# Kernel optimization log

Hardware: AMD Instinct MI355X
Metric: run time of the kernel (lower is better)

Reference implementation:

```python
import jax, jax.numpy as jnp
import numpy as np

N_HEADS = 16

def setup_inputs() -> dict:
    key = jax.random.key(0)
    ks = jax.random.split(key, 6)
    B, T, C = 8, 1024, 1024
    x = jax.random.normal(ks[0], (B, T, C), dtype=jnp.float32)
    s = 0.02
    Wk = jax.random.normal(ks[1], (C, C), dtype=jnp.float32) * s
    Wq = jax.random.normal(ks[2], (C, C), dtype=jnp.float32) * s
    Wv = jax.random.normal(ks[3], (C, C), dtype=jnp.float32) * s
    Wp = jax.random.normal(ks[4], (C, C), dtype=jnp.float32) * s
    bp = jax.random.normal(ks[5], (C,), dtype=jnp.float32) * s
    return {"x": x, "Wk": Wk, "Wq": Wq, "Wv": Wv, "Wp": Wp, "bp": bp}


def reference(x, Wk, Wq, Wv, Wp, bp):
    B, T, C = x.shape
    D = C // N_HEADS
    # torch Linear: y = x @ W^T
    def heads(W):
        h = (x @ W.T).reshape(B, T, N_HEADS, D)
        return jnp.transpose(h, (0, 2, 1, 3))  # [B,H,T,D]
    k, q, v = heads(Wk), heads(Wq), heads(Wv)
    # NOTE: source computes k @ q^T (rows index keys, cols index queries)
    att = jnp.einsum('bhid,bhjd->bhij', k, q) * (D ** -0.5)
    mask = jnp.tril(jnp.ones((T, T), dtype=bool))  # masked_fill where mask==0
    att = jnp.where(mask, att, -jnp.inf)
    att = jax.nn.softmax(att, axis=-1)
    y = jnp.einsum('bhij,bhjd->bhid', att, v)  # [B,H,T,D]
    y = jnp.transpose(y, (0, 2, 1, 3)).reshape(B, T, C)
    return y @ Wp.T + bp
```

## Files before the change

### kernel.cpp

```cpp
#include <hip/hip_runtime.h>
#include <hip/hip_bf16.h>


typedef __attribute__((ext_vector_type(8))) short short8;
typedef __attribute__((ext_vector_type(8))) unsigned short ushort8;
typedef __attribute__((ext_vector_type(4))) unsigned short ushort4_t;
typedef __attribute__((ext_vector_type(4))) unsigned int uintx4;
typedef __attribute__((ext_vector_type(4))) float floatx4;

#define LOG2E 1.44269504088896f

__device__ __forceinline__ unsigned short f2bf(float f) {
  unsigned int u = __float_as_uint(f);
  u += 0x7FFFu + ((u >> 16) & 1u);
  return (unsigned short)(u >> 16);
}

__device__ __forceinline__ unsigned int pack2bf(float lo, float hi) {
  return (unsigned int)f2bf(lo) | ((unsigned int)f2bf(hi) << 16);
}

__device__ __forceinline__ void gload_lds16(const void* g, void* l) {
  __builtin_amdgcn_global_load_lds(
      (const __attribute__((address_space(1))) unsigned int*)g,
      (__attribute__((address_space(3))) unsigned int*)l, 16, 0, 0);
}

__global__ __launch_bounds__(256) void cast_all_kernel(
    const float* __restrict__ x, const float* __restrict__ Wk,
    const float* __restrict__ Wq, const float* __restrict__ Wv,
    const float* __restrict__ Wp, unsigned short* __restrict__ xb,
    unsigned short* __restrict__ wb) {
  int idx = blockIdx.x * 256 + threadIdx.x;
  for (int i = idx; i < 1572864; i += 2048 * 256) {
    const float* src;
    unsigned short* dst;
    if (i < 1048576) {
      src = x + (size_t)i * 8;
      dst = xb + (size_t)i * 8;
    } else {
      int j = i - 1048576;
      int sel = j >> 17;
      int o = (j & 131071) * 8;
      const float* wsrc = sel == 0 ? Wk : sel == 1 ? Wq : sel == 2 ? Wv : Wp;
      src = wsrc + o;
      dst = wb + (size_t)sel * 1048576 + o;
    }
    const float4* p = reinterpret_cast<const float4*>(src);
    float4 a = p[0], b = p[1];
    ushort8 r;
    r[0] = f2bf(a.x); r[1] = f2bf(a.y); r[2] = f2bf(a.z); r[3] = f2bf(a.w);
    r[4] = f2bf(b.x); r[5] = f2bf(b.y); r[6] = f2bf(b.z); r[7] = f2bf(b.w);
    *reinterpret_cast<ushort8*>(dst) = r;
  }
}

template <int MODE, int NB>
__global__ __launch_bounds__(256) void gemm3_kernel(
    const unsigned short* __restrict__ A, const unsigned short* __restrict__ Bb,
    unsigned short* __restrict__ outb, float* __restrict__ outf,
    const float* __restrict__ bias) {
  const int tid = threadIdx.x;
  const int lane = tid & 63;
  const int w = tid >> 6;
  const int wr = w >> 1, wc = w & 1;
  const int g = lane >> 4, r = lane & 15;

  constexpr int NWG = NB * 64;
  constexpr int CPX = NWG / 8;
  const int bid = blockIdx.x;
  const int wgid = (bid & 7) * CPX + (bid >> 3);
  const int mb = wgid / NB, nb = wgid % NB;
  const int m0 = mb * 128, n0 = nb * 128;

  __shared__ unsigned short sA[3][128 * 32];
  __shared__ unsigned short sB[3][128 * 32];

  floatx4 acc[4][4];
#pragma unroll
  for (int i = 0; i < 4; ++i)
#pragma unroll
    for (int j = 0; j < 4; ++j) acc[i][j] = (floatx4)0.0f;

  const int srow = w * 16 + (lane >> 2);
  const int sc = (lane & 3) ^ ((lane >> 2) & 3);
  const char* gA0 = (const char*)(A + (size_t)(m0 + srow) * 1024) + sc * 16;
  const char* gA1 = (const char*)(A + (size_t)(m0 + 64 + srow) * 1024) + sc * 16;
  const char* gB0 = (const char*)(Bb + (size_t)(n0 + srow) * 1024) + sc * 16;
  const char* gB1 = (const char*)(Bb + (size_t)(n0 + 64 + srow) * 1024) + sc * 16;

  auto stage = [&](int bsel, int kt) {
    const size_t off = (size_t)kt * 64;
    gload_lds16(gA0 + off, &sA[bsel][(w * 16) * 32]);
    gload_lds16(gA1 + off, &sA[bsel][(64 + w * 16) * 32]);
    gload_lds16(gB0 + off, &sB[bsel][(w * 16) * 32]);
    gload_lds16(gB1 + off, &sB[bsel][(64 + w * 16) * 32]);
  };

  stage(0, 0);
  stage(1, 1);
  asm volatile("s_waitcnt vmcnt(4)" ::: "memory");
  __builtin_amdgcn_sched_barrier(0);
  __builtin_amdgcn_s_barrier();

  int bcur = 0;
  for (int kt = 0; kt < 32; ++kt) {
    if (kt < 30) {
      stage(bcur == 0 ? 2 : bcur - 1, kt + 2);
      asm volatile("s_waitcnt vmcnt(8)" ::: "memory");
    } else if (kt == 30) {
      asm volatile("s_waitcnt vmcnt(4)" ::: "memory");
    } else {
      asm volatile("s_waitcnt vmcnt(0)" ::: "memory");
    }
    __builtin_amdgcn_sched_barrier(0);

    short8 aF[4], bF[4];
#pragma unroll
    for (int mf = 0; mf < 4; ++mf) {
      const int row = wr * 64 + mf * 16 + r;
      aF[mf] = *reinterpret_cast<const short8*>(
          &sA[bcur][row * 32 + ((g ^ (r & 3)) * 8)]);
    }
#pragma unroll
    for (int nf = 0; nf < 4; ++nf) {
      const int row = wc * 64 + nf * 16 + r;
      bF[nf] = *reinterpret_cast<const short8*>(
          &sB[bcur][row * 32 + ((g ^ (r & 3)) * 8)]);
    }
#pragma unroll
    for (int mf = 0; mf < 4; ++mf)
#pragma unroll
      for (int nf = 0; nf < 4; ++nf)
        acc[mf][nf] = __builtin_amdgcn_mfma_f32_16x16x32_bf16(
            aF[mf], bF[nf], acc[mf][nf], 0, 0, 0);

    asm volatile("s_waitcnt lgkmcnt(0)" ::: "memory");
    __builtin_amdgcn_sched_barrier(0);
    __builtin_amdgcn_s_barrier();
    bcur = (bcur == 2) ? 0 : bcur + 1;
  }

  if (MODE == 0) {
    const int zB = n0 >> 10;
    unsigned short* outz = outb + (size_t)zB * 8388608;
    if (zB == 2) {
#pragma unroll
      for (int mf = 0; mf < 4; ++mf)
#pragma unroll
        for (int nf = 0; nf < 4; ++nf) {
          int m = m0 + wr * 64 + mf * 16 + g * 4;
          int nn = n0 + wc * 64 + nf * 16 + r;
          int b = m >> 10, t = m & 1023, h = (nn & 1023) >> 6, d = nn & 63;
          ushort4_t pk;
          pk[0] = f2bf(acc[mf][nf][0]); pk[1] = f2bf(acc[mf][nf][1]);
          pk[2] = f2bf(acc[mf][nf][2]); pk[3] = f2bf(acc[mf][nf][3]);
          *reinterpret_cast<ushort4_t*>(
              &outz[((size_t)((b * 16 + h) * 64 + d)) * 1024 + t]) = pk;
        }
    } else {
#pragma unroll
      for (int mf = 0; mf < 4; ++mf)
#pragma unroll
        for (int nf = 0; nf < 4; ++nf)
#pragma unroll
          for (int q = 0; q < 4; ++q) {
            int m = m0 + wr * 64 + mf * 16 + g * 4 + q;
            int nn = n0 + wc * 64 + nf * 16 + r;
            int b = m >> 10, t = m & 1023, h = (nn & 1023) >> 6, d = nn & 63;
            outz[(size_t)((b * 16 + h) * 1024 + t) * 64 + d] = f2bf(acc[mf][nf][q]);
          }
    }
  } else {
#pragma unroll
    for (int mf = 0; mf < 4; ++mf)
#pragma unroll
      for (int nf = 0; nf < 4; ++nf) {
        int nn = n0 + wc * 64 + nf * 16 + r;
        float bv = bias[nn];
#pragma unroll
        for (int q = 0; q < 4; ++q) {
          int m = m0 + wr * 64 + mf * 16 + g * 4 + q;
          outf[(size_t)m * 1024 + nn] = acc[mf][nf][q] + bv;
        }
      }
  }
}

__device__ __forceinline__ void softmax_pv_tile(
    floatx4 (&sT)[4], const unsigned short* __restrict__ Vb,
    floatx4 (&accYT)[4], float& m_run, float& l_run,
    int g, int r, int j0, int i_lane, bool diag) {
#pragma unroll
  for (int jf = 0; jf < 4; ++jf)
#pragma unroll
    for (int q = 0; q < 4; ++q) {
      float v = sT[jf][q] * 0.125f;
      if (diag && (j0 + jf * 16 + g * 4 + q > i_lane)) v = -1e30f;
      sT[jf][q] = v;
    }
  float mx = sT[0][0];
#pragma unroll
  for (int jf = 0; jf < 4; ++jf)
#pragma unroll
    for (int q = 0; q < 4; ++q) mx = fmaxf(mx, sT[jf][q]);
  mx = fmaxf(mx, __shfl_xor(mx, 16));
  mx = fmaxf(mx, __shfl_xor(mx, 32));
  float mnew = fmaxf(m_run, mx);
  float corr = exp2f((m_run - mnew) * LOG2E);
  m_run = mnew;
  float ssum = 0.0f;
#pragma unroll
  for (int jf = 0; jf < 4; ++jf)
#pragma unroll
    for (int q = 0; q < 4; ++q) {
      float p = exp2f((sT[jf][q] - mnew) * LOG2E);
      sT[jf][q] = p;
      ssum += p;
    }
  ssum += __shfl_xor(ssum, 16);
  ssum += __shfl_xor(ssum, 32);
  l_run = l_run * corr + ssum;
#pragma unroll
  for (int df = 0; df < 4; ++df) accYT[df] *= corr;
  unsigned int pk[4][2];
#pragma unroll
  for (int jf = 0; jf < 4; ++jf) {
    pk[jf][0] = pack2bf(sT[jf][0], sT[jf][1]);
    pk[jf][1] = pack2bf(sT[jf][2], sT[jf][3]);
  }
  short8 bP[2];
#pragma unroll
  for (int s = 0; s < 2; ++s) {
    uintx4 wd;
#pragma unroll
    for (int w_ = 0; w_ < 4; ++w_) {
      int src = (((g & 1) * 2 + (w_ >> 1)) << 4) + r;
      unsigned int t0 = (unsigned int)__shfl((int)pk[2 * s][w_ & 1], src);
      unsigned int t1 = (unsigned int)__shfl((int)pk[2 * s + 1][w_ & 1], src);
      wd[w_] = (g & 2) ? t1 : t0;
    }
    bP[s] = __builtin_bit_cast(short8, wd);
  }
  __builtin_amdgcn_s_setprio(1);
#pragma unroll
  for (int df = 0; df < 4; ++df) {
#pragma unroll
    for (int s = 0; s < 2; ++s) {
      short8 av = *reinterpret_cast<const short8*>(
          &Vb[(df * 16 + r) * 64 + ((s * 32 + g * 8) ^ ((r & 7) * 8))]);
      accYT[df] = __builtin_amdgcn_mfma_f32_16x16x32_bf16(av, bP[s], accYT[df], 0, 0, 0);
    }
  }
  __builtin_amdgcn_s_setprio(0);
}

__global__ __launch_bounds__(256, 4) void attn_kernel(
    const unsigned short* __restrict__ kqv, unsigned short* __restrict__ y) {
  const int tid = threadIdx.x;
  const int lane = tid & 63;
  const int w = tid >> 6;
  const int g = lane >> 4, r = lane & 15;
  const int bh = blockIdx.y;
  const int z = blockIdx.x;
  const int itA = z, itB = 15 - z;
  const int iwA = itA * 64 + w * 16;
  const int iwB = itB * 64 + w * 16;

  const unsigned short* Kh = kqv + (size_t)bh * 65536;
  const unsigned short* Qh = kqv + 8388608u + (size_t)bh * 65536;
  const unsigned short* Vt = kqv + 16777216u + (size_t)bh * 65536;

  __shared__ unsigned short Qs[2][64 * 64];
  __shared__ unsigned short Vs[2][64 * 64];

  short8 bKA[2], bKB[2];
#pragma unroll
  for (int s = 0; s < 2; ++s) {
    bKA[s] = *reinterpret_cast<const short8*>(&Kh[(size_t)(iwA + r) * 64 + s * 32 + g * 8]);
    bKB[s] = *reinterpret_cast<const short8*>(&Kh[(size_t)(iwB + r) * 64 + s * 32 + g * 8]);
  }

  floatx4 accA[4], accB[4];
#pragma unroll
  for (int df = 0; df < 4; ++df) { accA[df] = (floatx4)0.0f; accB[df] = (floatx4)0.0f; }
  float mA = -1e30f, lA = 0.0f, mB = -1e30f, lB = 0.0f;

  auto stage = [&](int bsel, int jts) {
    const int j0s = jts * 64;
    const int c = lane & 7;
#pragma unroll
    for (int u = 0; u < 2; ++u) {
      const int R = w * 16 + u * 8 + (lane >> 3);
      const int cc = c ^ (R & 7);
      gload_lds16(&Qh[(size_t)(j0s + R) * 64 + cc * 8], &Qs[bsel][(w * 16 + u * 8) * 64]);
      gload_lds16(&Vt[(size_t)R * 1024 + j0s + cc * 8], &Vs[bsel][(w * 16 + u * 8) * 64]);
    }
  };

  int buf = 0;
  stage(0, 0);
  __syncthreads();

  for (int jt = 0; jt <= itB; ++jt) {
    const int j0 = jt * 64;
    if (jt < itB) stage(buf ^ 1, jt + 1);

    const unsigned short* Qb = &Qs[buf][0];
    const unsigned short* Vb = &Vs[buf][0];

    floatx4 sT[4];
    __builtin_amdgcn_s_setprio(1);
#pragma unroll
    for (int jf = 0; jf < 4; ++jf) {
      sT[jf] = (floatx4)0.0f;
#pragma unroll
      for (int s = 0; s < 2; ++s) {
        short8 aq = *reinterpret_cast<const short8*>(
            &Qb[(jf * 16 + r) * 64 + ((s * 32 + g * 8) ^ ((r & 7) * 8))]);
        sT[jf] = __builtin_amdgcn_mfma_f32_16x16x32_bf16(aq, bKB[s], sT[jf], 0, 0, 0);
      }
    }
    __builtin_amdgcn_s_setprio(0);
    softmax_pv_tile(sT, Vb, accB, mB, lB, g, r, j0, iwB + r, jt == itB);

    if (jt <= itA) {
      floatx4 sA2[4];
      __builtin_amdgcn_s_setprio(1);
#pragma unroll
      for (int jf = 0; jf < 4; ++jf) {
        sA2[jf] = (floatx4)0.0f;
#pragma unroll
        for (int s = 0; s < 2; ++s) {
          short8 aq = *reinterpret_cast<const short8*>(
              &Qb[(jf * 16 + r) * 64 + ((s * 32 + g * 8) ^ ((r & 7) * 8))]);
          sA2[jf] = __builtin_amdgcn_mfma_f32_16x16x32_bf16(aq, bKA[s], sA2[jf], 0, 0, 0);
        }
      }
      __builtin_amdgcn_s_setprio(0);
      softmax_pv_tile(sA2, Vb, accA, mA, lA, g, r, j0, iwA + r, jt == itA);
    }

    __syncthreads();
    buf ^= 1;
  }

  const int b = bh >> 4, h = bh & 15;
#pragma unroll
  for (int tile = 0; tile < 2; ++tile) {
    const floatx4* acc = tile ? accB : accA;
    const float inv = 1.0f / (tile ? lB : lA);
    const int t = (tile ? iwB : iwA) + r;
    unsigned short* row = y + (size_t)(b * 1024 + t) * 1024 + h * 64;
#pragma unroll
    for (int df = 0; df < 4; ++df) {
      ushort4_t pkv;
      pkv[0] = f2bf(acc[df][0] * inv);
      pkv[1] = f2bf(acc[df][1] * inv);
      pkv[2] = f2bf(acc[df][2] * inv);
      pkv[3] = f2bf(acc[df][3] * inv);
      *reinterpret_cast<ushort4_t*>(&row[df * 16 + g * 4]) = pkv;
    }
  }
}

extern "C" void kernel_launch(void* const* d_in, const int* in_sizes, int n_in,
                              void* d_out, int out_size, void* d_ws, size_t ws_size,
                              hipStream_t stream) {
  const float* x  = (const float*)d_in[0];
  const float* Wk = (const float*)d_in[1];
  const float* Wq = (const float*)d_in[2];
  const float* Wv = (const float*)d_in[3];
  const float* Wp = (const float*)d_in[4];
  const float* bp = (const float*)d_in[5];
  float* out = (float*)d_out;

  char* ws = (char*)d_ws;
  unsigned short* xb  = (unsigned short*)ws;
  unsigned short* wb  = (unsigned short*)(ws + (16u << 20));
  unsigned short* kqv = (unsigned short*)(ws + (24u << 20));

  cast_all_kernel<<<2048, 256, 0, stream>>>(x, Wk, Wq, Wv, Wp, xb, wb);

  gemm3_kernel<0, 24><<<1536, 256, 0, stream>>>(xb, wb, kqv, nullptr, nullptr);

  attn_kernel<<<dim3(8, 128), 256, 0, stream>>>(kqv, xb );

  gemm3_kernel<1, 8><<<512, 256, 0, stream>>>(xb, wb + 3 * 1048576, nullptr, out, bp);
}
```

Measured before the change: 263.6 us.

## Use 256x128 tiles with 8 waves and a 4-slot half-K pipeline in GEMMs

The projection GEMMs move from 128x128 tiles with 4 waves to 256x128 tiles with 8 waves per block, so each B tile loaded into LDS is shared by twice as many rows. The K loop is split into 32-wide half steps staged through a 4-slot LDS ring with a single barrier per step, a new read swizzle, and s_setprio around the MFMA bursts. This targets global and LDS traffic per FLOP and the cost of synchronisation. In exchange it adds more LDS per block and halves the grid size, which may lower occupancy. The epilogue indexing (wr, wc) may not cover the larger tile correctly.

Result: slower. 275.8 us (+4.6%).

```diff
diff --git a/kernel.cpp b/kernel.cpp
--- a/kernel.cpp
+++ b/kernel.cpp
@@ -56,7 +56,7 @@
 }
 
 template <int MODE, int NB>
-__global__ __launch_bounds__(256) void gemm3_kernel(
+__global__ __launch_bounds__(512) void gemm4_kernel(
     const unsigned short* __restrict__ A, const unsigned short* __restrict__ Bb,
     unsigned short* __restrict__ outb, float* __restrict__ outf,
     const float* __restrict__ bias) {
@@ -65,16 +65,17 @@
   const int w = tid >> 6;
   const int wr = w >> 1, wc = w & 1;
   const int g = lane >> 4, r = lane & 15;
-
-  constexpr int NWG = NB * 64;
+  const int rdoff = ((g ^ ((r >> 1) & 3)) << 3);
+
+  constexpr int NWG = 32 * NB;
   constexpr int CPX = NWG / 8;
   const int bid = blockIdx.x;
   const int wgid = (bid & 7) * CPX + (bid >> 3);
   const int mb = wgid / NB, nb = wgid % NB;
-  const int m0 = mb * 128, n0 = nb * 128;
-
-  __shared__ unsigned short sA[3][128 * 32];
-  __shared__ unsigned short sB[3][128 * 32];
+  const int m0 = mb * 256, n0 = nb * 128;
+
+  __shared__ unsigned short sA[4][8192];
+  __shared__ unsigned short sB[4][4096];
 
   floatx4 acc[4][4];
 #pragma unroll
@@ -83,63 +84,66 @@
     for (int j = 0; j < 4; ++j) acc[i][j] = (floatx4)0.0f;
 
   const int srow = w * 16 + (lane >> 2);
-  const int sc = (lane & 3) ^ ((lane >> 2) & 3);
-  const char* gA0 = (const char*)(A + (size_t)(m0 + srow) * 1024) + sc * 16;
-  const char* gA1 = (const char*)(A + (size_t)(m0 + 64 + srow) * 1024) + sc * 16;
-  const char* gB0 = (const char*)(Bb + (size_t)(n0 + srow) * 1024) + sc * 16;
-  const char* gB1 = (const char*)(Bb + (size_t)(n0 + 64 + srow) * 1024) + sc * 16;
-
-  auto stage = [&](int bsel, int kt) {
-    const size_t off = (size_t)kt * 64;
-    gload_lds16(gA0 + off, &sA[bsel][(w * 16) * 32]);
-    gload_lds16(gA1 + off, &sA[bsel][(64 + w * 16) * 32]);
-    gload_lds16(gB0 + off, &sB[bsel][(w * 16) * 32]);
-    gload_lds16(gB1 + off, &sB[bsel][(64 + w * 16) * 32]);
+  const int scs = (lane & 3) ^ ((srow >> 1) & 3);
+  const unsigned short* gA0 = A + (size_t)(m0 + srow) * 1024 + scs * 8;
+  const unsigned short* gA1 = gA0 + 128 * 1024;
+  const unsigned short* gB0 = Bb + (size_t)(n0 + srow) * 1024 + scs * 8;
+
+  auto stage = [&](int P) {
+    const int slot = P & 3;
+    const int koff = (P >> 1) * 64 + (P & 1) * 32;
+    gload_lds16(gA0 + koff, &sA[slot][w * 512]);
+    gload_lds16(gA1 + koff, &sA[slot][4096 + w * 512]);
+    gload_lds16(gB0 + koff, &sB[slot][w * 512]);
   };
 
-  stage(0, 0);
-  stage(1, 1);
-  asm volatile("s_waitcnt vmcnt(4)" ::: "memory");
-  __builtin_amdgcn_sched_barrier(0);
-  __builtin_amdgcn_s_barrier();
-
-  int bcur = 0;
-  for (int kt = 0; kt < 32; ++kt) {
-    if (kt < 30) {
-      stage(bcur == 0 ? 2 : bcur - 1, kt + 2);
-      asm volatile("s_waitcnt vmcnt(8)" ::: "memory");
-    } else if (kt == 30) {
-      asm volatile("s_waitcnt vmcnt(4)" ::: "memory");
-    } else {
-      asm volatile("s_waitcnt vmcnt(0)" ::: "memory");
-    }
+  auto compute = [&](int P) {
+    const int slot = P & 3;
+    short8 aF[4], bF[4];
+#pragma unroll
+    for (int mf = 0; mf < 4; ++mf)
+      aF[mf] = *reinterpret_cast<const short8*>(
+          &sA[slot][(wr * 64 + mf * 16 + r) * 32 + rdoff]);
+#pragma unroll
+    for (int nf = 0; nf < 4; ++nf)
+      bF[nf] = *reinterpret_cast<const short8*>(
+          &sB[slot][(wc * 64 + nf * 16 + r) * 32 + rdoff]);
+    asm volatile("s_waitcnt lgkmcnt(0)" ::: "memory");
     __builtin_amdgcn_sched_barrier(0);
-
-    short8 aF[4], bF[4];
-#pragma unroll
-    for (int mf = 0; mf < 4; ++mf) {
-      const int row = wr * 64 + mf * 16 + r;
-      aF[mf] = *reinterpret_cast<const short8*>(
-          &sA[bcur][row * 32 + ((g ^ (r & 3)) * 8)]);
-    }
-#pragma unroll
-    for (int nf = 0; nf < 4; ++nf) {
-      const int row = wc * 64 + nf * 16 + r;
-      bF[nf] = *reinterpret_cast<const short8*>(
-          &sB[bcur][row * 32 + ((g ^ (r & 3)) * 8)]);
-    }
+    __builtin_amdgcn_s_setprio(1);
 #pragma unroll
     for (int mf = 0; mf < 4; ++mf)
 #pragma unroll
       for (int nf = 0; nf < 4; ++nf)
         acc[mf][nf] = __builtin_amdgcn_mfma_f32_16x16x32_bf16(
             aF[mf], bF[nf], acc[mf][nf], 0, 0, 0);
-
-    asm volatile("s_waitcnt lgkmcnt(0)" ::: "memory");
+    __builtin_amdgcn_s_setprio(0);
+  };
+
+  stage(0); stage(1); stage(2);
+  for (int P = 0; P < 29; ++P) {
+    asm volatile("s_waitcnt vmcnt(6)" ::: "memory");
     __builtin_amdgcn_sched_barrier(0);
     __builtin_amdgcn_s_barrier();
-    bcur = (bcur == 2) ? 0 : bcur + 1;
-  }
+    __builtin_amdgcn_sched_barrier(0);
+    stage(P + 3);
+    compute(P);
+  }
+  asm volatile("s_waitcnt vmcnt(6)" ::: "memory");
+  __builtin_amdgcn_sched_barrier(0);
+  __builtin_amdgcn_s_barrier();
+  __builtin_amdgcn_sched_barrier(0);
+  compute(29);
+  asm volatile("s_waitcnt vmcnt(3)" ::: "memory");
+  __builtin_amdgcn_sched_barrier(0);
+  __builtin_amdgcn_s_barrier();
+  __builtin_amdgcn_sched_barrier(0);
+  compute(30);
+  asm volatile("s_waitcnt vmcnt(0)" ::: "memory");
+  __builtin_amdgcn_sched_barrier(0);
+  __builtin_amdgcn_s_barrier();
+  __builtin_amdgcn_sched_barrier(0);
+  compute(31);
 
   if (MODE == 0) {
     const int zB = n0 >> 10;
@@ -382,9 +386,9 @@
 
   cast_all_kernel<<<2048, 256, 0, stream>>>(x, Wk, Wq, Wv, Wp, xb, wb);
 
-  gemm3_kernel<0, 24><<<1536, 256, 0, stream>>>(xb, wb, kqv, nullptr, nullptr);
+  gemm4_kernel<0, 24><<<768, 512, 0, stream>>>(xb, wb, kqv, nullptr, nullptr);
 
   attn_kernel<<<dim3(8, 128), 256, 0, stream>>>(kqv, xb );
 
-  gemm3_kernel<1, 8><<<512, 256, 0, stream>>>(xb, wb + 3 * 1048576, nullptr, out, bp);
-}
+  gemm4_kernel<1, 8><<<256, 512, 0, stream>>>(xb, wb + 3 * 1048576, nullptr, out, bp);
+}
```
